# Kernel optimization log

Hardware: AMD Instinct MI355X
Metric: run time of the kernel (lower is better)

## Reference

```python
import jax, jax.numpy as jnp
import numpy as np

LAG = 5
MSG_HID = 256
N_ATOMS = 30
N_EDGES = N_ATOMS * (N_ATOMS - 1)  # 870
BATCH = 2
T = 200


def _rel_matrices():
    # fully-connected directed graph, no self loops (standard NRI encoding)
    recv, send = [], []
    for i in range(N_ATOMS):
        for j in range(N_ATOMS):
            if i != j:
                recv.append(i)
                send.append(j)
    rel_rec = np.zeros((N_EDGES, N_ATOMS), dtype=np.float32)
    rel_send = np.zeros((N_EDGES, N_ATOMS), dtype=np.float32)
    rel_rec[np.arange(N_EDGES), recv] = 1.0
    rel_send[np.arange(N_EDGES), send] = 1.0
    return jnp.asarray(rel_rec), jnp.asarray(rel_send)


def setup_inputs() -> dict:
    key = jax.random.key(0)
    ks = jax.random.split(key, 14)
    rel_rec, rel_send = _rel_matrices()
    s = 0.05
    return {
        "inputs": jax.random.normal(ks[0], (BATCH, N_ATOMS, T), jnp.float32),
        "mu": jax.random.normal(ks[1], (BATCH, N_EDGES), jnp.float32),
        "logvar": jax.random.normal(ks[2], (BATCH, N_EDGES), jnp.float32) * 0.1,
        "eps": jax.random.normal(ks[3], (BATCH, N_EDGES), jnp.float32),
        "rel_rec": rel_rec,
        "rel_send": rel_send,
        "w_msg1": jax.random.normal(ks[4], (2 * LAG, MSG_HID), jnp.float32) * s,
        "b_msg1": jnp.zeros((MSG_HID,), jnp.float32),
        "w_msg2": jax.random.normal(ks[5], (MSG_HID, MSG_HID), jnp.float32) * s,
        "b_msg2": jnp.zeros((MSG_HID,), jnp.float32),
        "w_out1": jax.random.normal(ks[6], (LAG + MSG_HID, MSG_HID), jnp.float32) * s,
        "b_out1": jnp.zeros((MSG_HID,), jnp.float32),
        "w_out2": jax.random.normal(ks[7], (MSG_HID, MSG_HID), jnp.float32) * s,
        "b_out2": jnp.zeros((MSG_HID,), jnp.float32),
        "w_out3": jax.random.normal(ks[8], (MSG_HID, 1), jnp.float32) * s,
        "b_out3": jnp.zeros((1,), jnp.float32),
    }


def reference(inputs, mu, logvar, eps, rel_rec, rel_send,
              w_msg1, b_msg1, w_msg2, b_msg2,
              w_out1, b_out1, w_out2, b_out2, w_out3, b_out3):
    # reparametrize: edges [B, E]
    edges = eps * jnp.exp(0.5 * logvar) + mu

    # lag-stack: data [B, T-lag, N, lag]
    Tm = inputs.shape[2] - LAG
    data = jnp.stack([inputs[:, :, i:i + Tm] for i in range(LAG)], axis=-1)
    data = jnp.transpose(data, (0, 2, 1, 3))  # [B, Tm, N, lag]

    # gather node features to edges via one-hot matmuls
    receivers = jnp.einsum('en,btnl->btel', rel_rec, data)   # [B, Tm, E, lag]
    senders = jnp.einsum('en,btnl->btel', rel_send, data)    # [B, Tm, E, lag]
    pre_msg = jnp.concatenate([senders, receivers], axis=-1)  # [B, Tm, E, 2*lag]

    msg = jax.nn.relu(pre_msg @ w_msg1 + b_msg1)
    msg = jax.nn.relu(msg @ w_msg2 + b_msg2)                 # [B, Tm, E, hid]
    msg = msg * edges[:, None, :, None]                       # edge mask

    # scatter-aggregate messages back to receiver nodes
    agg_msgs = jnp.einsum('bteh,en->btnh', msg, rel_rec)      # [B, Tm, N, hid]

    aug = jnp.concatenate([data, agg_msgs], axis=-1)          # [B, Tm, N, lag+hid]
    pred = jax.nn.relu(aug @ w_out1 + b_out1)
    pred = jax.nn.relu(pred @ w_out2 + b_out2)
    pred = (pred @ w_out3 + b_out3)[..., 0]                   # [B, Tm, N]

    return jnp.transpose(pred, (0, 2, 1))                     # [B, N, Tm]
```

## Files before the change

### kernel.cpp

```cpp
#include <hip/hip_runtime.h>

#define LAG 5
#define HID 256
#define NA 30
#define NE 870
#define TM 195
#define TT 200
#define NB 2
#define EPN 29
#define TB2 98
#define NROWS (NB * TM * NA)
#define APAD 4
#define KC 32
#define UVB 1463
#define W2F_ELEMS (HID * HID)
#define W1F_ELEMS (HID * 288)
#define NWG2 (NB * NA * TB2)
#define Q8 (NWG2 / 8)

typedef _Float16 f16;
typedef _Float16 f16x8 __attribute__((ext_vector_type(8)));
typedef float floatx4 __attribute__((ext_vector_type(4)));
typedef float floatx16 __attribute__((ext_vector_type(16)));

__global__ __launch_bounds__(256) void k1_prep(
    const float* __restrict__ inputs, const float* __restrict__ w_msg1,
    const float* __restrict__ b_msg1, const float* __restrict__ w_msg2,
    const float* __restrict__ w_out1, const float* __restrict__ w_out2,
    f16* __restrict__ u, f16* __restrict__ v, f16* __restrict__ w2frag,
    f16* __restrict__ w1frag, f16* __restrict__ w2ofrag)
{
    const int bid = blockIdx.x, tid = threadIdx.x;
    if (bid < UVB) {
        __shared__ float feats8[8][LAG];
        const int r0 = bid * 8;
        if (tid < 8 * LAG) {
            const int i = tid / LAG, l = tid % LAG;
            const int r = r0 + i;
            float fv = 0.f;
            if (r < NROWS) {
                const int b = r / (TM * NA), rem = r % (TM * NA);
                const int t = rem / NA, n = rem % NA;
                fv = inputs[(b * NA + n) * TT + t + l];
            }
            feats8[i][l] = fv;
        }
        float w1c[2 * LAG];
        #pragma unroll
        for (int k = 0; k < 2 * LAG; ++k) w1c[k] = w_msg1[k * HID + tid];
        const float bb = b_msg1[tid];
        __syncthreads();
        const int c = tid >> 3, e = tid & 7;
        #pragma unroll
        for (int i = 0; i < 8; ++i) {
            const int r = r0 + i;
            if (r < NROWS) {
                float ua = bb, va = 0.f;
                #pragma unroll
                for (int l = 0; l < LAG; ++l) {
                    ua = fmaf(feats8[i][l], w1c[l], ua);
                    va = fmaf(feats8[i][l], w1c[LAG + l], va);
                }
                const int b = r / (TM * NA), rem = r % (TM * NA);
                const int t = rem / NA, n = rem % NA;
                const int base = ((b * TM + t) * 32 + c) * 240 + n * 8 + e;
                u[base] = (f16)ua;
                v[base] = (f16)va;
            }
        }
    } else if (bid < UVB + 32) {
        const int fidx = (bid - UVB) * 256 + tid;
        const int lane = fidx & 63;
        const int kc = (fidx >> 6) & 15;
        const int c32 = fidx >> 10;
        const int col = c32 * 32 + (lane & 31);
        const int kb = kc * 16 + (lane >> 5) * 8;
        f16x8 vv;
        #pragma unroll
        for (int x = 0; x < 8; ++x) vv[x] = (f16)w_msg2[(kb + x) * HID + col];
        *(f16x8*)&w2frag[fidx * 8] = vv;
    } else if (bid < UVB + 32 + 36) {
        const int fidx = (bid - (UVB + 32)) * 256 + tid;
        const int lane = fidx & 63;
        const int kc = (fidx >> 6) % 9;
        const int ntc = fidx / (64 * 9);
        const int col = ntc * 16 + (lane & 15);
        const int kb = kc * KC + (lane >> 4) * 8;
        f16x8 vv;
        #pragma unroll
        for (int x = 0; x < 8; ++x) {
            const int k = kb + x;
            float val;
            if (k < 256)      val = w_out1[(5 + k) * HID + col];
            else if (k < 261) val = w_out1[(k - 256) * HID + col];
            else              val = 0.f;
            vv[x] = (f16)val;
        }
        *(f16x8*)&w1frag[fidx * 8] = vv;
    } else {
        const int fidx = (bid - (UVB + 32 + 36)) * 256 + tid;
        const int lane = fidx & 63;
        const int kc = (fidx >> 6) & 7;
        const int ntc = fidx >> 9;
        const int col = ntc * 16 + (lane & 15);
        const int kb = kc * KC + (lane >> 4) * 8;
        f16x8 vv;
        #pragma unroll
        for (int x = 0; x < 8; ++x) vv[x] = (f16)w_out2[(kb + x) * HID + col];
        *(f16x8*)&w2ofrag[fidx * 8] = vv;
    }
}

__global__ __launch_bounds__(256, 3) void k2_msg(
    const f16* __restrict__ u, const f16* __restrict__ v,
    const f16* __restrict__ w2frag,
    const float* __restrict__ mu, const float* __restrict__ logvar,
    const float* __restrict__ eps, const float* __restrict__ b_msg2,
    f16* __restrict__ agg)
{
    __shared__ f16 a_lds[32 * 64 * 8];
    __shared__ float ev_lds[32];

    const int bid0 = blockIdx.x;
    const int bid = (bid0 & 7) * Q8 + (bid0 >> 3);

    const int n  = bid % NA;
    const int tb = (bid / NA) % TB2;
    const int b  = bid / (NA * TB2);
    const int t0 = tb * 2;
    const int tid = threadIdx.x;
    const int lane = tid & 63, w = tid >> 6;
    const int h = lane >> 5, l31 = lane & 31;

    if (tid < 32) {
        float evv = 0.f;
        if (tid < EPN) {
            const int e = b * NE + n * EPN + tid;
            evv = eps[e] * __expf(0.5f * logvar[e]) + mu[e];
        }
        ev_lds[tid] = evv;
    }

    const f16x8 z8 = {(f16)0, (f16)0, (f16)0, (f16)0, (f16)0, (f16)0, (f16)0, (f16)0};

    #pragma unroll
    for (int i = 0; i < 8; ++i) {
        const int task = i * 256 + tid;
        const int frag = task >> 6, fl = task & 63;
        const int tt = frag >> 4, kc = frag & 15;
        const int hh = fl >> 5, ei = fl & 31;
        const int c = kc * 2 + hh;
        const int t = t0 + tt;
        f16x8 out8 = z8;
        if (ei < EPN && t < TM) {
            const int rowbase = ((b * TM + t) * 32 + c) * 240;
            const int j = ei + (ei >= n);
            const f16x8 uu = *(const f16x8*)(u + rowbase + j * 8);
            const f16x8 vv = *(const f16x8*)(v + rowbase + n * 8);
            out8 = __builtin_elementwise_max(uu + vv, z8);
        }
        *(f16x8*)&a_lds[task * 8] = out8;
    }

    const f16* bb[2];
    bb[0] = w2frag + (((2 * w + 0) * 16) << 9) + (lane << 3);
    bb[1] = w2frag + (((2 * w + 1) * 16) << 9) + (lane << 3);
    f16x8 b0[2], b1[2];
    #pragma unroll
    for (int nt = 0; nt < 2; ++nt) {
        b0[nt] = *(const f16x8*)(bb[nt] + (0 << 9));
        b1[nt] = *(const f16x8*)(bb[nt] + (1 << 9));
    }

    floatx16 acc[2][2];
    #pragma unroll
    for (int tt = 0; tt < 2; ++tt)
        #pragma unroll
        for (int nt = 0; nt < 2; ++nt)
            #pragma unroll
            for (int x = 0; x < 16; ++x) acc[tt][nt][x] = 0.f;

    __syncthreads();

    #pragma unroll
    for (int kc = 0; kc < 16; ++kc) {
        f16x8 b2[2];
        #pragma unroll
        for (int nt = 0; nt < 2; ++nt) {
            b2[nt] = b1[nt];
            if (kc < 14) b2[nt] = *(const f16x8*)(bb[nt] + ((kc + 2) << 9));
        }
        f16x8 af[2];
        #pragma unroll
        for (int tt = 0; tt < 2; ++tt)
            af[tt] = *(const f16x8*)&a_lds[((tt * 16 + kc) * 64 + lane) * 8];
        __builtin_amdgcn_s_setprio(1);
        #pragma unroll
        for (int nt = 0; nt < 2; ++nt)
            #pragma unroll
            for (int tt = 0; tt < 2; ++tt)
                acc[tt][nt] = __builtin_amdgcn_mfma_f32_32x32x16_f16(af[tt], b0[nt], acc[tt][nt], 0, 0, 0);
        __builtin_amdgcn_s_setprio(0);
        #pragma unroll
        for (int nt = 0; nt < 2; ++nt) { b0[nt] = b1[nt]; b1[nt] = b2[nt]; }
    }

    float evr[16];
    #pragma unroll
    for (int reg = 0; reg < 16; ++reg)
        evr[reg] = ev_lds[(reg & 3) + 8 * (reg >> 2) + 4 * h];
    float b2s[2];
    #pragma unroll
    for (int nt = 0; nt < 2; ++nt) b2s[nt] = b_msg2[(2 * w + nt) * 32 + l31];

    #pragma unroll
    for (int tt = 0; tt < 2; ++tt) {
        const int t = t0 + tt;
        #pragma unroll
        for (int nt = 0; nt < 2; ++nt) {
            float part = 0.f;
            #pragma unroll
            for (int reg = 0; reg < 16; ++reg)
                part += evr[reg] * fmaxf(acc[tt][nt][reg] + b2s[nt], 0.f);
            part += __shfl_xor(part, 32, 64);
            if (h == 0 && t < TM)
                agg[(((b * TM + t) * NA + n) << 8) + (2 * w + nt) * 32 + l31] = (f16)part;
        }
    }
}

__global__ __launch_bounds__(256) void k3_out(
    const f16* __restrict__ agg, const float* __restrict__ inputs,
    const f16* __restrict__ w1frag, const f16* __restrict__ w2ofrag,
    const float* __restrict__ b_out1, const float* __restrict__ b_out2,
    const float* __restrict__ w_out3, const float* __restrict__ b_out3,
    float* __restrict__ out)
{
    __shared__ f16 a1[16][288 + APAD];
    __shared__ float red[4][16];

    const int R0 = blockIdx.x * 16;
    const int tid = threadIdx.x;
    const int lane = tid & 63, w = tid >> 6;
    const int q = lane >> 4, m15 = lane & 15;
    const int wbase = w * 64;

    #pragma unroll
    for (int i = 0; i < 2; ++i) {
        const int task = i * 256 + tid;
        const int row = task >> 5, c = task & 31;
        const int R = R0 + row;
        f16x8 val;
        if (R < NROWS) {
            val = *(const f16x8*)&agg[(R << 8) + c * 8];
        } else {
            for (int x = 0; x < 8; ++x) val[x] = (f16)0.f;
        }
        *(f16x8*)&a1[row][c * 8] = val;
    }
    if (tid < 16) {
        const int R = R0 + tid;
        if (R < NROWS) {
            const int b = R / (TM * NA), rem = R % (TM * NA);
            const int t = rem / NA, n = rem % NA;
            const float* ip = inputs + (b * NA + n) * TT + t;
            #pragma unroll
            for (int l = 0; l < LAG; ++l) a1[tid][256 + l] = (f16)ip[l];
            #pragma unroll
            for (int k = 261; k < 288; ++k) a1[tid][k] = (f16)0.f;
        } else {
            for (int k = 256; k < 288; ++k) a1[tid][k] = (f16)0.f;
        }
    }

    floatx4 acc[4];
    #pragma unroll
    for (int nt = 0; nt < 4; ++nt) acc[nt] = (floatx4){0.f, 0.f, 0.f, 0.f};

    const f16* b1base = w1frag + (lane << 3);
    f16x8 bcur[4], bnxt[4];
    #pragma unroll
    for (int nt = 0; nt < 4; ++nt)
        bcur[nt] = *(const f16x8*)(b1base + (((w * 4 + nt) * 9 + 0) << 9));

    __syncthreads();

    #pragma unroll
    for (int kc = 0; kc < 9; ++kc) {
        if (kc < 8) {
            #pragma unroll
            for (int nt = 0; nt < 4; ++nt)
                bnxt[nt] = *(const f16x8*)(b1base + (((w * 4 + nt) * 9 + kc + 1) << 9));
        }
        const f16x8 af = *(const f16x8*)&a1[m15][kc * KC + q * 8];
        #pragma unroll
        for (int nt = 0; nt < 4; ++nt)
            acc[nt] = __builtin_amdgcn_mfma_f32_16x16x32_f16(af, bcur[nt], acc[nt], 0, 0, 0);
        #pragma unroll
        for (int nt = 0; nt < 4; ++nt) bcur[nt] = bnxt[nt];
    }
    __syncthreads();

    {
        float b1v[4];
        #pragma unroll
        for (int nt = 0; nt < 4; ++nt) b1v[nt] = b_out1[wbase + nt * 16 + m15];
        #pragma unroll
        for (int nt = 0; nt < 4; ++nt)
            #pragma unroll
            for (int reg = 0; reg < 4; ++reg)
                a1[q * 4 + reg][wbase + nt * 16 + m15] =
                    (f16)fmaxf(acc[nt][reg] + b1v[nt], 0.f);
    }

    #pragma unroll
    for (int nt = 0; nt < 4; ++nt) acc[nt] = (floatx4){0.f, 0.f, 0.f, 0.f};

    const f16* b2base = w2ofrag + (lane << 3);
    #pragma unroll
    for (int nt = 0; nt < 4; ++nt)
        bcur[nt] = *(const f16x8*)(b2base + (((w * 4 + nt) * 8 + 0) << 9));

    __syncthreads();

    #pragma unroll
    for (int kc = 0; kc < 8; ++kc) {
        if (kc < 7) {
            #pragma unroll
            for (int nt = 0; nt < 4; ++nt)
                bnxt[nt] = *(const f16x8*)(b2base + (((w * 4 + nt) * 8 + kc + 1) << 9));
        }
        const f16x8 af = *(const f16x8*)&a1[m15][kc * KC + q * 8];
        #pragma unroll
        for (int nt = 0; nt < 4; ++nt)
            acc[nt] = __builtin_amdgcn_mfma_f32_16x16x32_f16(af, bcur[nt], acc[nt], 0, 0, 0);
        #pragma unroll
        for (int nt = 0; nt < 4; ++nt) bcur[nt] = bnxt[nt];
    }

    {
        float b2v[4], w3v[4];
        #pragma unroll
        for (int nt = 0; nt < 4; ++nt) {
            const int col = wbase + nt * 16 + m15;
            b2v[nt] = b_out2[col];
            w3v[nt] = w_out3[col];
        }
        #pragma unroll
        for (int reg = 0; reg < 4; ++reg) {
            float p = 0.f;
            #pragma unroll
            for (int nt = 0; nt < 4; ++nt)
                p += fmaxf(acc[nt][reg] + b2v[nt], 0.f) * w3v[nt];
            p += __shfl_xor(p, 1, 64);
            p += __shfl_xor(p, 2, 64);
            p += __shfl_xor(p, 4, 64);
            p += __shfl_xor(p, 8, 64);
            if (m15 == 0) red[w][q * 4 + reg] = p;
        }
    }
    __syncthreads();
    if (tid < 16) {
        const int R = R0 + tid;
        if (R < NROWS) {
            const float val = red[0][tid] + red[1][tid] + red[2][tid] + red[3][tid] + b_out3[0];
            const int b = R / (TM * NA), rem = R % (TM * NA);
            const int t = rem / NA, n = rem % NA;
            out[(b * NA + n) * TM + t] = val;
        }
    }
}

extern "C" void kernel_launch(void* const* d_in, const int* in_sizes, int n_in,
                              void* d_out, int out_size, void* d_ws, size_t ws_size,
                              hipStream_t stream) {
    const float* inputs  = (const float*)d_in[0];
    const float* mu      = (const float*)d_in[1];
    const float* logvar  = (const float*)d_in[2];
    const float* eps     = (const float*)d_in[3];
    const float* w_msg1  = (const float*)d_in[6];
    const float* b_msg1  = (const float*)d_in[7];
    const float* w_msg2  = (const float*)d_in[8];
    const float* b_msg2  = (const float*)d_in[9];
    const float* w_out1  = (const float*)d_in[10];
    const float* b_out1  = (const float*)d_in[11];
    const float* w_out2  = (const float*)d_in[12];
    const float* b_out2  = (const float*)d_in[13];
    const float* w_out3  = (const float*)d_in[14];
    const float* b_out3  = (const float*)d_in[15];
    float* out = (float*)d_out;

    f16* u       = (f16*)d_ws;
    f16* v       = u       + NROWS * HID;
    f16* aggw    = v       + NROWS * HID;
    f16* w2frag  = aggw    + NROWS * HID;
    f16* w1frag  = w2frag  + W2F_ELEMS;
    f16* w2ofrag = w1frag  + W1F_ELEMS;

    hipLaunchKernelGGL(k1_prep, dim3(UVB + 32 + 36 + 32), dim3(256), 0, stream,
                       inputs, w_msg1, b_msg1, w_msg2, w_out1, w_out2,
                       u, v, w2frag, w1frag, w2ofrag);
    hipLaunchKernelGGL(k2_msg, dim3(NWG2), dim3(256), 0, stream,
                       u, v, w2frag, mu, logvar, eps, b_msg2, aggw);
    hipLaunchKernelGGL(k3_out, dim3((NROWS + 15) / 16), dim3(256), 0, stream,
                       aggw, inputs, w1frag, w2ofrag, b_out1, b_out2, w_out3, b_out3, out);
}
```

Before: 164.2 us.

## Restructure u/v prep per time slab, overlap A staging with MFMA, double k3 rows

```diff
diff --git a/kernel.cpp b/kernel.cpp
--- a/kernel.cpp
+++ b/kernel.cpp
@@ -12,7 +12,7 @@
 #define NROWS (NB * TM * NA)
 #define APAD 4
 #define KC 32
-#define UVB 1463
+#define UVSLABS (NB * TM)
 #define W2F_ELEMS (HID * HID)
 #define W1F_ELEMS (HID * 288)
 #define NWG2 (NB * NA * TB2)
@@ -31,45 +31,40 @@
     f16* __restrict__ w1frag, f16* __restrict__ w2ofrag)
 {
     const int bid = blockIdx.x, tid = threadIdx.x;
-    if (bid < UVB) {
-        __shared__ float feats8[8][LAG];
-        const int r0 = bid * 8;
-        if (tid < 8 * LAG) {
-            const int i = tid / LAG, l = tid % LAG;
-            const int r = r0 + i;
-            float fv = 0.f;
-            if (r < NROWS) {
-                const int b = r / (TM * NA), rem = r % (TM * NA);
-                const int t = rem / NA, n = rem % NA;
-                fv = inputs[(b * NA + n) * TT + t + l];
-            }
-            feats8[i][l] = fv;
-        }
-        float w1c[2 * LAG];
-        #pragma unroll
-        for (int k = 0; k < 2 * LAG; ++k) w1c[k] = w_msg1[k * HID + tid];
-        const float bb = b_msg1[tid];
+    if (bid < UVSLABS) {
+        __shared__ float w1_lds[10 * 256];
+        __shared__ float b1_lds[256];
+        __shared__ float feats[30 * 5];
+        const int b = bid / TM, t = bid % TM;
+        #pragma unroll
+        for (int i = 0; i < 10; ++i) w1_lds[i * 256 + tid] = w_msg1[i * 256 + tid];
+        b1_lds[tid] = b_msg1[tid];
+        if (tid < 150) {
+            const int n = tid / 5, l = tid % 5;
+            feats[tid] = inputs[(b * NA + n) * TT + t + l];
+        }
         __syncthreads();
-        const int c = tid >> 3, e = tid & 7;
-        #pragma unroll
-        for (int i = 0; i < 8; ++i) {
-            const int r = r0 + i;
-            if (r < NROWS) {
-                float ua = bb, va = 0.f;
+        if (tid < 240) {
+            const int n = tid >> 3;
+            float fr[LAG];
+            #pragma unroll
+            for (int l = 0; l < LAG; ++l) fr[l] = feats[n * 5 + l];
+            const int slab = (b * TM + t) * (32 * 240);
+            #pragma unroll 4
+            for (int c = 0; c < 32; ++c) {
+                const int col = c * 8 + (tid & 7);
+                float ua = b1_lds[col], va = 0.f;
                 #pragma unroll
                 for (int l = 0; l < LAG; ++l) {
-                    ua = fmaf(feats8[i][l], w1c[l], ua);
-                    va = fmaf(feats8[i][l], w1c[LAG + l], va);
+                    ua = fmaf(fr[l], w1_lds[l * 256 + col], ua);
+                    va = fmaf(fr[l], w1_lds[(LAG + l) * 256 + col], va);
                 }
-                const int b = r / (TM * NA), rem = r % (TM * NA);
-                const int t = rem / NA, n = rem % NA;
-                const int base = ((b * TM + t) * 32 + c) * 240 + n * 8 + e;
-                u[base] = (f16)ua;
-                v[base] = (f16)va;
+                u[slab + c * 240 + tid] = (f16)ua;
+                v[slab + c * 240 + tid] = (f16)va;
             }
         }
-    } else if (bid < UVB + 32) {
-        const int fidx = (bid - UVB) * 256 + tid;
+    } else if (bid < UVSLABS + 32) {
+        const int fidx = (bid - UVSLABS) * 256 + tid;
         const int lane = fidx & 63;
         const int kc = (fidx >> 6) & 15;
         const int c32 = fidx >> 10;
@@ -79,8 +74,8 @@
         #pragma unroll
         for (int x = 0; x < 8; ++x) vv[x] = (f16)w_msg2[(kb + x) * HID + col];
         *(f16x8*)&w2frag[fidx * 8] = vv;
-    } else if (bid < UVB + 32 + 36) {
-        const int fidx = (bid - (UVB + 32)) * 256 + tid;
+    } else if (bid < UVSLABS + 32 + 36) {
+        const int fidx = (bid - (UVSLABS + 32)) * 256 + tid;
         const int lane = fidx & 63;
         const int kc = (fidx >> 6) % 9;
         const int ntc = fidx / (64 * 9);
@@ -98,7 +93,7 @@
         }
         *(f16x8*)&w1frag[fidx * 8] = vv;
     } else {
-        const int fidx = (bid - (UVB + 32 + 36)) * 256 + tid;
+        const int fidx = (bid - (UVSLABS + 32 + 36)) * 256 + tid;
         const int lane = fidx & 63;
         const int kc = (fidx >> 6) & 7;
         const int ntc = fidx >> 9;
@@ -111,7 +106,7 @@
     }
 }
 
-__global__ __launch_bounds__(256, 3) void k2_msg(
+__global__ __launch_bounds__(256, 4) void k2_msg(
     const f16* __restrict__ u, const f16* __restrict__ v,
     const f16* __restrict__ w2frag,
     const float* __restrict__ mu, const float* __restrict__ logvar,
@@ -143,13 +138,12 @@
 
     const f16x8 z8 = {(f16)0, (f16)0, (f16)0, (f16)0, (f16)0, (f16)0, (f16)0, (f16)0};
 
-    #pragma unroll
-    for (int i = 0; i < 8; ++i) {
+    auto stage_iter = [&](int i) {
         const int task = i * 256 + tid;
         const int frag = task >> 6, fl = task & 63;
-        const int tt = frag >> 4, kc = frag & 15;
+        const int tt = frag >> 4, kcs = frag & 15;
         const int hh = fl >> 5, ei = fl & 31;
-        const int c = kc * 2 + hh;
+        const int c = kcs * 2 + hh;
         const int t = t0 + tt;
         f16x8 out8 = z8;
         if (ei < EPN && t < TM) {
@@ -160,7 +154,10 @@
             out8 = __builtin_elementwise_max(uu + vv, z8);
         }
         *(f16x8*)&a_lds[task * 8] = out8;
-    }
+    };
+
+    #pragma unroll
+    for (int s = 0; s < 4; ++s) stage_iter(s < 2 ? s : s + 2);
 
     const f16* bb[2];
     bb[0] = w2frag + (((2 * w + 0) * 16) << 9) + (lane << 3);
@@ -183,7 +180,34 @@
     __syncthreads();
 
     #pragma unroll
-    for (int kc = 0; kc < 16; ++kc) {
+    for (int kc = 0; kc < 8; ++kc) {
+        f16x8 b2[2];
+        #pragma unroll
+        for (int nt = 0; nt < 2; ++nt)
+            b2[nt] = *(const f16x8*)(bb[nt] + ((kc + 2) << 9));
+        f16x8 af[2];
+        #pragma unroll
+        for (int tt = 0; tt < 2; ++tt)
+            af[tt] = *(const f16x8*)&a_lds[((tt * 16 + kc) * 64 + lane) * 8];
+        __builtin_amdgcn_s_setprio(1);
+        #pragma unroll
+        for (int nt = 0; nt < 2; ++nt)
+            #pragma unroll
+            for (int tt = 0; tt < 2; ++tt)
+                acc[tt][nt] = __builtin_amdgcn_mfma_f32_32x32x16_f16(af[tt], b0[nt], acc[tt][nt], 0, 0, 0);
+        __builtin_amdgcn_s_setprio(0);
+        #pragma unroll
+        for (int nt = 0; nt < 2; ++nt) { b0[nt] = b1[nt]; b1[nt] = b2[nt]; }
+        if ((kc & 1) == 0) {
+            const int half = kc >> 1;
+            stage_iter(half < 2 ? half + 2 : half + 4);
+        }
+    }
+
+    __syncthreads();
+
+    #pragma unroll
+    for (int kc = 8; kc < 16; ++kc) {
         f16x8 b2[2];
         #pragma unroll
         for (int nt = 0; nt < 2; ++nt) {
@@ -236,17 +260,17 @@
     const float* __restrict__ w_out3, const float* __restrict__ b_out3,
     float* __restrict__ out)
 {
-    __shared__ f16 a1[16][288 + APAD];
-    __shared__ float red[4][16];
-
-    const int R0 = blockIdx.x * 16;
+    __shared__ f16 a1[32][288 + APAD];
+    __shared__ float red[4][32];
+
+    const int R0 = blockIdx.x * 32;
     const int tid = threadIdx.x;
     const int lane = tid & 63, w = tid >> 6;
     const int q = lane >> 4, m15 = lane & 15;
     const int wbase = w * 64;
 
     #pragma unroll
-    for (int i = 0; i < 2; ++i) {
+    for (int i = 0; i < 4; ++i) {
         const int task = i * 256 + tid;
         const int row = task >> 5, c = task & 31;
         const int R = R0 + row;
@@ -258,7 +282,7 @@
         }
         *(f16x8*)&a1[row][c * 8] = val;
     }
-    if (tid < 16) {
+    if (tid < 32) {
         const int R = R0 + tid;
         if (R < NROWS) {
             const int b = R / (TM * NA), rem = R % (TM * NA);
@@ -273,9 +297,11 @@
         }
     }
 
-    floatx4 acc[4];
-    #pragma unroll
-    for (int nt = 0; nt < 4; ++nt) acc[nt] = (floatx4){0.f, 0.f, 0.f, 0.f};
+    floatx4 acc[2][4];
+    #pragma unroll
+    for (int ms = 0; ms < 2; ++ms)
+        #pragma unroll
+        for (int nt = 0; nt < 4; ++nt) acc[ms][nt] = (floatx4){0.f, 0.f, 0.f, 0.f};
 
     const f16* b1base = w1frag + (lane << 3);
     f16x8 bcur[4], bnxt[4];
@@ -292,10 +318,15 @@
             for (int nt = 0; nt < 4; ++nt)
                 bnxt[nt] = *(const f16x8*)(b1base + (((w * 4 + nt) * 9 + kc + 1) << 9));
         }
-        const f16x8 af = *(const f16x8*)&a1[m15][kc * KC + q * 8];
+        f16x8 af[2];
+        #pragma unroll
+        for (int ms = 0; ms < 2; ++ms)
+            af[ms] = *(const f16x8*)&a1[ms * 16 + m15][kc * KC + q * 8];
         #pragma unroll
         for (int nt = 0; nt < 4; ++nt)
-            acc[nt] = __builtin_amdgcn_mfma_f32_16x16x32_f16(af, bcur[nt], acc[nt], 0, 0, 0);
+            #pragma unroll
+            for (int ms = 0; ms < 2; ++ms)
+                acc[ms][nt] = __builtin_amdgcn_mfma_f32_16x16x32_f16(af[ms], bcur[nt], acc[ms][nt], 0, 0, 0);
         #pragma unroll
         for (int nt = 0; nt < 4; ++nt) bcur[nt] = bnxt[nt];
     }
@@ -306,15 +337,19 @@
         #pragma unroll
         for (int nt = 0; nt < 4; ++nt) b1v[nt] = b_out1[wbase + nt * 16 + m15];
         #pragma unroll
-        for (int nt = 0; nt < 4; ++nt)
-            #pragma unroll
-            for (int reg = 0; reg < 4; ++reg)
-                a1[q * 4 + reg][wbase + nt * 16 + m15] =
-                    (f16)fmaxf(acc[nt][reg] + b1v[nt], 0.f);
-    }
-
-    #pragma unroll
-    for (int nt = 0; nt < 4; ++nt) acc[nt] = (floatx4){0.f, 0.f, 0.f, 0.f};
+        for (int ms = 0; ms < 2; ++ms)
+            #pragma unroll
+            for (int nt = 0; nt < 4; ++nt)
+                #pragma unroll
+                for (int reg = 0; reg < 4; ++reg)
+                    a1[ms * 16 + q * 4 + reg][wbase + nt * 16 + m15] =
+                        (f16)fmaxf(acc[ms][nt][reg] + b1v[nt], 0.f);
+    }
+
+    #pragma unroll
+    for (int ms = 0; ms < 2; ++ms)
+        #pragma unroll
+        for (int nt = 0; nt < 4; ++nt) acc[ms][nt] = (floatx4){0.f, 0.f, 0.f, 0.f};
 
     const f16* b2base = w2ofrag + (lane << 3);
     #pragma unroll
@@ -330,10 +365,15 @@
             for (int nt = 0; nt < 4; ++nt)
                 bnxt[nt] = *(const f16x8*)(b2base + (((w * 4 + nt) * 8 + kc + 1) << 9));
         }
-        const f16x8 af = *(const f16x8*)&a1[m15][kc * KC + q * 8];
+        f16x8 af[2];
+        #pragma unroll
+        for (int ms = 0; ms < 2; ++ms)
+            af[ms] = *(const f16x8*)&a1[ms * 16 + m15][kc * KC + q * 8];
         #pragma unroll
         for (int nt = 0; nt < 4; ++nt)
-            acc[nt] = __builtin_amdgcn_mfma_f32_16x16x32_f16(af, bcur[nt], acc[nt], 0, 0, 0);
+            #pragma unroll
+            for (int ms = 0; ms < 2; ++ms)
+                acc[ms][nt] = __builtin_amdgcn_mfma_f32_16x16x32_f16(af[ms], bcur[nt], acc[ms][nt], 0, 0, 0);
         #pragma unroll
         for (int nt = 0; nt < 4; ++nt) bcur[nt] = bnxt[nt];
     }
@@ -347,20 +387,22 @@
             w3v[nt] = w_out3[col];
         }
         #pragma unroll
-        for (int reg = 0; reg < 4; ++reg) {
-            float p = 0.f;
-            #pragma unroll
-            for (int nt = 0; nt < 4; ++nt)
-                p += fmaxf(acc[nt][reg] + b2v[nt], 0.f) * w3v[nt];
-            p += __shfl_xor(p, 1, 64);
-            p += __shfl_xor(p, 2, 64);
-            p += __shfl_xor(p, 4, 64);
-            p += __shfl_xor(p, 8, 64);
-            if (m15 == 0) red[w][q * 4 + reg] = p;
-        }
-    }
-    __syncthreads();
-    if (tid < 16) {
+        for (int ms = 0; ms < 2; ++ms)
+            #pragma unroll
+            for (int reg = 0; reg < 4; ++reg) {
+                float p = 0.f;
+                #pragma unroll
+                for (int nt = 0; nt < 4; ++nt)
+                    p += fmaxf(acc[ms][nt][reg] + b2v[nt], 0.f) * w3v[nt];
+                p += __shfl_xor(p, 1, 64);
+                p += __shfl_xor(p, 2, 64);
+                p += __shfl_xor(p, 4, 64);
+                p += __shfl_xor(p, 8, 64);
+                if (m15 == 0) red[w][ms * 16 + q * 4 + reg] = p;
+            }
+    }
+    __syncthreads();
+    if (tid < 32) {
         const int R = R0 + tid;
         if (R < NROWS) {
             const float val = red[0][tid] + red[1][tid] + red[2][tid] + red[3][tid] + b_out3[0];
@@ -397,11 +439,11 @@
     f16* w1frag  = w2frag  + W2F_ELEMS;
     f16* w2ofrag = w1frag  + W1F_ELEMS;
 
-    hipLaunchKernelGGL(k1_prep, dim3(UVB + 32 + 36 + 32), dim3(256), 0, stream,
+    hipLaunchKernelGGL(k1_prep, dim3(UVSLABS + 32 + 36 + 32), dim3(256), 0, stream,
                        inputs, w_msg1, b_msg1, w_msg2, w_out1, w_out2,
                        u, v, w2frag, w1frag, w2ofrag);
     hipLaunchKernelGGL(k2_msg, dim3(NWG2), dim3(256), 0, stream,
                        u, v, w2frag, mu, logvar, eps, b_msg2, aggw);
-    hipLaunchKernelGGL(k3_out, dim3((NROWS + 15) / 16), dim3(256), 0, stream,
+    hipLaunchKernelGGL(k3_out, dim3((NROWS + 31) / 32), dim3(256), 0, stream,
                        aggw, inputs, w1frag, w2ofrag, b_out1, b_out2, w_out3, b_out3, out);
 }
```

Result: no change. 165.0 us (+0.5%).
